# Kernel tuning notes

Measured on AMD Instinct MI355X. Metric: run time of the kernel, lower is better.

Reference implementation:

```python
import jax, jax.numpy as jnp
import numpy as np

ALPHA = 0.2  # LeakyReLU slope
EPS = 1e-16


def _spgat_layer(x, W, a, row, col, N, concat):
    # h: [N, d]
    h = x @ W
    d = h.shape[1]
    # edge attention: a^T [h_row || h_col]  (pyGAT SpGAT: exp(-leakyrelu(.)))
    f_src = h @ a[:d]   # [N]
    f_dst = h @ a[d:]   # [N]
    e = jnp.exp(-jax.nn.leaky_relu(f_src[row] + f_dst[col], ALPHA))  # [E]
    denom = jax.ops.segment_sum(e, row, num_segments=N) + EPS        # [N]
    num = jax.ops.segment_sum(e[:, None] * h[col], row, num_segments=N)  # [N, d]
    out = num / denom[:, None]
    return jax.nn.elu(out) if concat else out


def _spgat(x, W1, a1, W2, a2, edges):
    row, col = edges[0], edges[1]
    N = x.shape[0]
    h = _spgat_layer(x, W1, a1, row, col, N, concat=True)
    h = _spgat_layer(h, W2, a2, row, col, N, concat=False)
    return jax.nn.elu(h)


def setup_inputs() -> dict:
    key = jax.random.key(0)
    ks = jax.random.split(key, 20)
    VOCAB, NFEAT = 50000, 300
    N_TW, L = 50000, 16
    UV = 50000
    E = 800000
    HID, JOINT, NCLASS = 64, 128, 2
    B = 4096

    inp = {}
    # integer structure (constants)
    inp['features_index'] = jax.random.randint(ks[0], (N_TW, L), 0, VOCAB, dtype=jnp.int32)
    inp['tw_edges'] = jax.random.randint(ks[1], (2, E), 0, N_TW, dtype=jnp.int32)
    inp['ut_edges'] = jax.random.randint(ks[2], (2, E), 0, UV, dtype=jnp.int32)
    inp['tw_graph_idx'] = jax.random.randint(ks[3], (B,), 0, N_TW, dtype=jnp.int32)
    inp['ut_graph_idx'] = jax.random.randint(ks[4], (B,), 0, UV, dtype=jnp.int32)
    # learned parameters
    inp['word_emb'] = jax.random.normal(ks[5], (VOCAB, NFEAT), jnp.float32) * 0.1
    inp['user_emb'] = jax.random.normal(ks[6], (UV, NFEAT), jnp.float32) * 0.1
    def gat_params(k, din, dh, dout):
        k1, k2, k3, k4 = jax.random.split(k, 4)
        return (jax.random.normal(k1, (din, dh), jnp.float32) * (1.0 / np.sqrt(din)),
                jax.random.normal(k2, (2 * dh,), jnp.float32) * 0.1,
                jax.random.normal(k3, (dh, dout), jnp.float32) * (1.0 / np.sqrt(dh)),
                jax.random.normal(k4, (2 * dout,), jnp.float32) * 0.1)
    inp['tw_W1'], inp['tw_a1'], inp['tw_W2'], inp['tw_a2'] = gat_params(ks[7], NFEAT, HID, JOINT)
    inp['tu_W1'], inp['tu_a1'], inp['tu_W2'], inp['tu_a2'] = gat_params(ks[8], NFEAT, HID, JOINT)
    inp['weight_W'] = jax.random.uniform(ks[9], (JOINT, JOINT), jnp.float32, -0.1, 0.1)
    inp['weight_proj'] = jax.random.uniform(ks[10], (JOINT, 1), jnp.float32, -0.1, 0.1)
    inp['out_W'] = jax.random.normal(ks[11], (NCLASS, JOINT), jnp.float32) * (1.0 / np.sqrt(JOINT))
    inp['out_b'] = jnp.zeros((NCLASS,), jnp.float32)
    return inp


def reference(word_emb, user_emb, tw_W1, tw_a1, tw_W2, tw_a2,
              tu_W1, tu_a1, tu_W2, tu_a2, weight_W, weight_proj,
              out_W, out_b, features_index, tw_edges, ut_edges,
              tw_graph_idx, ut_graph_idx):
    # tweet features: mean of word embeddings per tweet  [N_tw, nfeat]
    twt_X = word_emb[features_index].mean(axis=1)
    tw_X = _spgat(twt_X, tw_W1, tw_a1, tw_W2, tw_a2, tw_edges)   # [N_tw, joint]
    tu_X = _spgat(user_emb, tu_W1, tu_a1, tu_W2, tu_a2, ut_edges)  # [uV, joint]
    # attention-weighted fusion of the two views
    u_tw = jnp.tanh(tw_X @ weight_W)
    u_tu = jnp.tanh(tu_X @ weight_W)
    att_tw = jnp.mean(u_tw @ weight_proj, axis=0)  # [1]
    att_tu = jnp.mean(u_tu @ weight_proj, axis=0)  # [1]
    att = jax.nn.softmax(jnp.concatenate([att_tw, att_tu], axis=0))  # [2]
    feat = att[0] * tw_X[tw_graph_idx] + att[1] * tu_X[ut_graph_idx]  # [B, joint]
    logits = feat @ out_W.T + out_b
    return jax.nn.log_softmax(logits, axis=1)
```

## Files before the change

kernel.cpp:

```cpp
#include <hip/hip_runtime.h>
#include <hip/hip_bf16.h>

typedef __hip_bfloat16 bf16;
typedef unsigned int uint32;
typedef __attribute__((ext_vector_type(8))) short s8v;
typedef __attribute__((ext_vector_type(4))) short s4v;
typedef __attribute__((ext_vector_type(8))) short bf8v;
typedef __attribute__((ext_vector_type(4))) float f4v;

#define CAP 64
#define CAPSH 6

__device__ __forceinline__ float waveReduce(float v) {
#pragma unroll
    for (int o = 32; o > 0; o >>= 1) v += __shfl_xor(v, o, 64);
    return v;
}

__device__ __forceinline__ short f2bf(float x) {
    __hip_bfloat16 h = __float2bfloat16(x);
    return *reinterpret_cast<short*>(&h);
}
__device__ __forceinline__ float bf2f(short s) {
    return __uint_as_float(((uint32)(unsigned short)s) << 16);
}
__device__ __forceinline__ uint32 pack2(float x, float y) {
    return (uint32)(unsigned short)f2bf(x) | (((uint32)(unsigned short)f2bf(y)) << 16);
}
__device__ __forceinline__ float blo(uint32 d) { return __uint_as_float(d << 16); }
__device__ __forceinline__ float bhi(uint32 d) { return __uint_as_float(d & 0xffff0000u); }
__device__ __forceinline__ float felu(float x) { return x > 0.f ? x : __expf(x) - 1.f; }

struct WJobs {
    const float* src[5];
    short* dst[5];
    int K[5], N[5], KP[5], total[5];
    int* cursor;
    float* attsum;
    int N2;
};
__global__ void wtrans_all(WJobs jb) {
    int j = blockIdx.y;
    int i = blockIdx.x * blockDim.x + threadIdx.x;
    if (j == 5) {
        if (i < jb.N2) jb.cursor[i] = i << CAPSH;
        if (i < 2) jb.attsum[i] = 0.f;
        return;
    }
    if (i >= jb.total[j]) return;
    int KP = jb.KP[j];
    int n = i / KP, k = i - n * KP;
    jb.dst[j][i] = f2bf(k < jb.K[j] ? jb.src[j][(size_t)k * jb.N[j] + n] : 0.f);
}

struct GJob {
    const void* A;
    const short* Wt;
    const float* av;
    void* C;
    float* fs;
    float* fd;
    int M;
};
struct SJob {
    const int* rowA; const int* colA;
    const int* rowB; const int* colB;
    int* cursor; int* ecol;
    int E; int NTW; int nbg; int Wsize;
};

template <typename AT, int K, int KPAD, int N, int CSTORE, bool DO_F, bool DO_ATT, bool DO_SCAT>
__global__ __launch_bounds__(256) void mfma_gemm(GJob j0, GJob j1, int nb0,
                                                 float* __restrict__ attsum, int bnd, SJob sj) {
    constexpr int NT = N / 16;
    constexpr int NP = KPAD / 64;
    int t = threadIdx.x;

    if constexpr (DO_SCAT) {
        if ((int)blockIdx.x >= sj.nbg) {
            int bb = (int)blockIdx.x - sj.nbg;
            int w = (int)blockIdx.x & 7;
            int i = (bb >> 3) * 256 + t;
            int lo = w * sj.Wsize;
            int hi = lo + sj.Wsize;
            int r = -1, c = 0;
            if (i < sj.E) {
                r = sj.rowA[i]; c = sj.colA[i];
            } else if (i < 2 * sj.E) {
                r = sj.NTW + sj.rowB[i - sj.E]; c = sj.colB[i - sj.E];
            }
            if (r >= lo && r < hi) {
                int p0 = atomicAdd(&sj.cursor[r], 1);
                if (p0 < (r << CAPSH) + CAP) sj.ecol[p0] = c;
            }
            return;
        }
    }

    __shared__ short As[64 * 72];
    __shared__ short Ws[N * 72];
    __shared__ float red[8];
    int lane = t & 63;
    int wid = t >> 6;
    int col = lane & 15;
    int quad = lane >> 4;

    int bid = blockIdx.x;
    bool sec = bid >= nb0;
    GJob J = sec ? j1 : j0;
    const AT* A = (const AT*)J.A;
    const short* Wt = J.Wt;
    const float* av = J.av;
    int M = J.M;
    int row0 = (sec ? bid - nb0 : bid) * 64;

    f4v acc[NT];
#pragma unroll
    for (int i = 0; i < NT; ++i) { f4v z = {0.f, 0.f, 0.f, 0.f}; acc[i] = z; }

    float4 ra[4];
    s8v rsa[2];
    s8v rb[NT / 2];

    auto issue = [&](int p) {
        int k0 = p * 64;
        if constexpr (sizeof(AT) == 4) {
            const float4* A4 = (const float4*)A;
            int f = t & 15, r0 = t >> 4;
#pragma unroll
            for (int r = 0; r < 4; ++r) {
                int gr = row0 + r0 + 16 * r;
                int f4i = (k0 >> 2) + f;
                float4 v = {0.f, 0.f, 0.f, 0.f};
                if (gr < M && f4i < K / 4) v = A4[(size_t)gr * (K / 4) + f4i];
                ra[r] = v;
            }
        } else {
            int c8 = t & 7, r0 = t >> 3;
#pragma unroll
            for (int r = 0; r < 2; ++r) {
                int gr = row0 + r0 + 32 * r;
                s8v v = {0, 0, 0, 0, 0, 0, 0, 0};
                if (gr < M) v = *(const s8v*)&A[(size_t)gr * K + k0 + c8 * 8];
                rsa[r] = v;
            }
        }
        {
            int c8 = t & 7, r0 = t >> 3;
#pragma unroll
            for (int r = 0; r < NT / 2; ++r)
                rb[r] = *(const s8v*)&Wt[(size_t)(r0 + 32 * r) * KPAD + k0 + c8 * 8];
        }
    };
    auto commit = [&]() {
        if constexpr (sizeof(AT) == 4) {
            int f = t & 15, r0 = t >> 4;
#pragma unroll
            for (int r = 0; r < 4; ++r) {
                float4 v = ra[r];
                s4v sv = {f2bf(v.x), f2bf(v.y), f2bf(v.z), f2bf(v.w)};
                *(s4v*)&As[(r0 + 16 * r) * 72 + f * 4] = sv;
            }
        } else {
            int c8 = t & 7, r0 = t >> 3;
#pragma unroll
            for (int r = 0; r < 2; ++r) *(s8v*)&As[(r0 + 32 * r) * 72 + c8 * 8] = rsa[r];
        }
        int c8 = t & 7, r0 = t >> 3;
#pragma unroll
        for (int r = 0; r < NT / 2; ++r) *(s8v*)&Ws[(r0 + 32 * r) * 72 + c8 * 8] = rb[r];
    };

    issue(0);
    for (int p = 0; p < NP; ++p) {
        __syncthreads();
        commit();
        __syncthreads();
        if (p + 1 < NP) issue(p + 1);
#pragma unroll
        for (int c2 = 0; c2 < 2; ++c2) {
            int ko = c2 * 32 + quad * 8;
            bf8v af = *(const bf8v*)&As[(wid * 16 + col) * 72 + ko];
#pragma unroll
            for (int nt = 0; nt < NT; ++nt) {
                bf8v bf = *(const bf8v*)&Ws[(nt * 16 + col) * 72 + ko];
                acc[nt] = __builtin_amdgcn_mfma_f32_16x16x32_bf16(af, bf, acc[nt], 0, 0, 0);
            }
        }
    }

    int mbase = row0 + wid * 16;
    if constexpr (CSTORE == 1) {
        float* C = (float*)J.C;
#pragma unroll
        for (int nt = 0; nt < NT; ++nt)
#pragma unroll
            for (int r = 0; r < 4; ++r) {
                int gr = mbase + quad * 4 + r;
                if (gr < M) C[(size_t)gr * N + nt * 16 + col] = acc[nt][r];
            }
    } else if constexpr (CSTORE == 2) {
        short* C = (short*)J.C;
#pragma unroll
        for (int nt = 0; nt < NT; ++nt)
#pragma unroll
            for (int r = 0; r < 4; ++r) {
                int gr = mbase + quad * 4 + r;
                if (gr < M) C[(size_t)gr * N + nt * 16 + col] = f2bf(acc[nt][r]);
            }
    }
    if constexpr (DO_F) {
        if (av) {
            float* fs = J.fs;
            float* fd = J.fd;
            float a0[NT], a1[NT];
#pragma unroll
            for (int nt = 0; nt < NT; ++nt) {
                a0[nt] = av[nt * 16 + col];
                a1[nt] = av[N + nt * 16 + col];
            }
#pragma unroll
            for (int r = 0; r < 4; ++r) {
                float p0 = 0.f, p1 = 0.f;
#pragma unroll
                for (int nt = 0; nt < NT; ++nt) {
                    p0 += acc[nt][r] * a0[nt];
                    p1 += acc[nt][r] * a1[nt];
                }
#pragma unroll
                for (int o = 8; o > 0; o >>= 1) {
                    p0 += __shfl_xor(p0, o, 64);
                    p1 += __shfl_xor(p1, o, 64);
                }
                int gr = mbase + quad * 4 + r;
                if (col == 0 && gr < M) { fs[gr] = p0; fd[gr] = p1; }
            }
        }
    }
    if constexpr (DO_ATT) {
        float s0 = 0.f, s1 = 0.f;
#pragma unroll
        for (int nt = 0; nt < NT; ++nt) {
            float pj = av[nt * 16 + col];
#pragma unroll
            for (int r = 0; r < 4; ++r) {
                int gr = mbase + quad * 4 + r;
                float v = tanhf(acc[nt][r]) * pj;
                if (gr < bnd) s0 += v; else s1 += v;
            }
        }
        s0 = waveReduce(s0);
        s1 = waveReduce(s1);
        if (lane == 0) { red[wid] = s0; red[4 + wid] = s1; }
        __syncthreads();
        if (t == 0) {
            atomicAdd(attsum + 0, red[0] + red[1] + red[2] + red[3]);
            atomicAdd(attsum + 1, red[4] + red[5] + red[6] + red[7]);
        }
    }
}

__global__ void gather_h64(const int* __restrict__ idx, const uint32* __restrict__ P,
                           const float* __restrict__ a,
                           short* __restrict__ H, float* __restrict__ fsv, float* __restrict__ fdv,
                           int N) {
    int wv = (blockIdx.x * blockDim.x + threadIdx.x) >> 6;
    int lane = threadIdx.x & 63;
    if (wv >= N) return;
    int hf = lane >> 5, li = lane & 31;
    const int* ip = idx + wv * 16;
    float a0 = 0.f, a1 = 0.f;
#pragma unroll
    for (int u = 0; u < 8; ++u) {
        int ind = ip[2 * u + hf];
        uint32 d = P[(size_t)ind * 32 + li];
        a0 += blo(d);
        a1 += bhi(d);
    }
    a0 += __shfl_xor(a0, 32, 64);
    a1 += __shfl_xor(a1, 32, 64);
    a0 *= 0.0625f;
    a1 *= 0.0625f;
    if (hf == 0) ((uint32*)H)[(size_t)wv * 32 + li] = pack2(a0, a1);
    float cp = hf ? 0.f : (a0 * a[2 * li] + a1 * a[2 * li + 1]);
    float cq = hf ? 0.f : (a0 * a[64 + 2 * li] + a1 * a[64 + 2 * li + 1]);
    float p = waveReduce(cp);
    float q = waveReduce(cq);
    if (lane == 0) { fsv[wv] = p; fdv[wv] = q; }
}

__global__ void agg64f_kernel(const int* __restrict__ cursor, const int* __restrict__ ecol,
                              const float* __restrict__ fs, const float* __restrict__ fd,
                              const uint32* __restrict__ hb, uint32* __restrict__ out,
                              int N2, int NTW) {
    int wv = (blockIdx.x * blockDim.x + threadIdx.x) >> 6;
    int lane = threadIdx.x & 63;
    if (wv >= N2) return;
    int s = wv << CAPSH;
    int ne = min(cursor[wv] - s, CAP);
    int coff = wv < NTW ? 0 : NTW;
    float fsr = fs[wv];
    int cl = 0;
    float el = 0.f;
    if (lane < ne) {
        cl = ecol[s + lane];
        float f = fsr + fd[coff + cl];
        el = __expf(-(f >= 0.f ? f : 0.2f * f));
    }
    int qd = lane >> 4, li = lane & 15;
    const uint2* h2 = (const uint2*)hb;
    float a0 = 0.f, a1 = 0.f, a2 = 0.f, a3 = 0.f, den = 0.f;
    for (int kb = 0; kb < ne; kb += 16) {
        int k0 = kb + qd, k1 = kb + 4 + qd, k2 = kb + 8 + qd, k3 = kb + 12 + qd;
        int c0 = __shfl(cl, k0, 64); float e0 = __shfl(el, k0, 64);
        int c1 = __shfl(cl, k1, 64); float e1 = __shfl(el, k1, 64);
        int c2 = __shfl(cl, k2, 64); float e2 = __shfl(el, k2, 64);
        int c3 = __shfl(cl, k3, 64); float e3 = __shfl(el, k3, 64);
        uint2 d0 = h2[(size_t)(coff + c0) * 16 + li];
        uint2 d1 = h2[(size_t)(coff + c1) * 16 + li];
        uint2 d2 = h2[(size_t)(coff + c2) * 16 + li];
        uint2 d3 = h2[(size_t)(coff + c3) * 16 + li];
        a0 += e0 * blo(d0.x) + e1 * blo(d1.x) + e2 * blo(d2.x) + e3 * blo(d3.x);
        a1 += e0 * bhi(d0.x) + e1 * bhi(d1.x) + e2 * bhi(d2.x) + e3 * bhi(d3.x);
        a2 += e0 * blo(d0.y) + e1 * blo(d1.y) + e2 * blo(d2.y) + e3 * blo(d3.y);
        a3 += e0 * bhi(d0.y) + e1 * bhi(d1.y) + e2 * bhi(d2.y) + e3 * bhi(d3.y);
        den += e0 + e1 + e2 + e3;
    }
    a0 += __shfl_xor(a0, 16, 64); a0 += __shfl_xor(a0, 32, 64);
    a1 += __shfl_xor(a1, 16, 64); a1 += __shfl_xor(a1, 32, 64);
    a2 += __shfl_xor(a2, 16, 64); a2 += __shfl_xor(a2, 32, 64);
    a3 += __shfl_xor(a3, 16, 64); a3 += __shfl_xor(a3, 32, 64);
    den += __shfl_xor(den, 16, 64); den += __shfl_xor(den, 32, 64);
    if (lane < 16) {
        float inv = 1.f / (den + 1e-16f);
        float v0 = felu(a0 * inv);
        float v1 = felu(a1 * inv);
        float v2 = felu(a2 * inv);
        float v3 = felu(a3 * inv);
        uint2 o = {pack2(v0, v1), pack2(v2, v3)};
        ((uint2*)out)[(size_t)wv * 16 + li] = o;
    }
}

__global__ void agg128f_kernel(const int* __restrict__ cursor, const int* __restrict__ ecol,
                               const float* __restrict__ fs, const float* __restrict__ fd,
                               const uint32* __restrict__ hb, uint32* __restrict__ out,
                               int N2, int NTW) {
    int wv = (blockIdx.x * blockDim.x + threadIdx.x) >> 6;
    int lane = threadIdx.x & 63;
    if (wv >= N2) return;
    int s = wv << CAPSH;
    int ne = min(cursor[wv] - s, CAP);
    int coff = wv < NTW ? 0 : NTW;
    float fsr = fs[wv];
    int cl = 0;
    float el = 0.f;
    if (lane < ne) {
        cl = ecol[s + lane];
        float f = fsr + fd[coff + cl];
        el = __expf(-(f >= 0.f ? f : 0.2f * f));
    }
    int hf = lane >> 5, li = lane & 31;
    const uint2* h2 = (const uint2*)hb;
    float a0 = 0.f, a1 = 0.f, a2 = 0.f, a3 = 0.f, den = 0.f;
    for (int kb = 0; kb < ne; kb += 8) {
        int k0 = kb + hf, k1 = kb + 2 + hf, k2 = kb + 4 + hf, k3 = kb + 6 + hf;
        int c0 = __shfl(cl, k0, 64); float e0 = __shfl(el, k0, 64);
        int c1 = __shfl(cl, k1, 64); float e1 = __shfl(el, k1, 64);
        int c2 = __shfl(cl, k2, 64); float e2 = __shfl(el, k2, 64);
        int c3 = __shfl(cl, k3, 64); float e3 = __shfl(el, k3, 64);
        uint2 d0 = h2[(size_t)(coff + c0) * 32 + li];
        uint2 d1 = h2[(size_t)(coff + c1) * 32 + li];
        uint2 d2 = h2[(size_t)(coff + c2) * 32 + li];
        uint2 d3 = h2[(size_t)(coff + c3) * 32 + li];
        a0 += e0 * blo(d0.x) + e1 * blo(d1.x) + e2 * blo(d2.x) + e3 * blo(d3.x);
        a1 += e0 * bhi(d0.x) + e1 * bhi(d1.x) + e2 * bhi(d2.x) + e3 * bhi(d3.x);
        a2 += e0 * blo(d0.y) + e1 * blo(d1.y) + e2 * blo(d2.y) + e3 * blo(d3.y);
        a3 += e0 * bhi(d0.y) + e1 * bhi(d1.y) + e2 * bhi(d2.y) + e3 * bhi(d3.y);
        den += e0 + e1 + e2 + e3;
    }
    a0 += __shfl_xor(a0, 32, 64);
    a1 += __shfl_xor(a1, 32, 64);
    a2 += __shfl_xor(a2, 32, 64);
    a3 += __shfl_xor(a3, 32, 64);
    den += __shfl_xor(den, 32, 64);
    if (hf == 0) {
        float inv = 1.f / (den + 1e-16f);
        float v0 = felu(a0 * inv);
        float v1 = felu(a1 * inv);
        float v2 = felu(a2 * inv);
        float v3 = felu(a3 * inv);
        uint2 o = {pack2(v0, v1), pack2(v2, v3)};
        ((uint2*)out)[(size_t)wv * 32 + li] = o;
    }
}

__global__ void final_kernel(const short* __restrict__ twX, const short* __restrict__ tuX,
                             const int* __restrict__ twi, const int* __restrict__ tui,
                             const float* __restrict__ attsum,
                             const float* __restrict__ outW, const float* __restrict__ outb,
                             float* __restrict__ out, int B, float invNtw, float invNuv) {
    int wave = (blockIdx.x * blockDim.x + threadIdx.x) >> 6;
    int lane = threadIdx.x & 63;
    if (wave >= B) return;
    float z0 = attsum[0] * invNtw, z1 = attsum[1] * invNuv;
    float m = fmaxf(z0, z1);
    float e0 = expf(z0 - m), e1 = expf(z1 - m);
    float a0 = e0 / (e0 + e1), a1 = e1 / (e0 + e1);
    int ti = twi[wave], ui = tui[wave];
    float l0 = 0.f, l1 = 0.f;
#pragma unroll
    for (int p = 0; p < 2; ++p) {
        int j = lane + 64 * p;
        float feat = a0 * bf2f(twX[(size_t)ti * 128 + j]) + a1 * bf2f(tuX[(size_t)ui * 128 + j]);
        l0 += feat * outW[j];
        l1 += feat * outW[128 + j];
    }
    l0 = waveReduce(l0);
    l1 = waveReduce(l1);
    if (lane == 0) {
        l0 += outb[0];
        l1 += outb[1];
        float mm = fmaxf(l0, l1);
        float lse = mm + logf(expf(l0 - mm) + expf(l1 - mm));
        out[wave * 2 + 0] = l0 - lse;
        out[wave * 2 + 1] = l1 - lse;
    }
}

extern "C" void kernel_launch(void* const* d_in, const int* in_sizes, int n_in,
                              void* d_out, int out_size, void* d_ws, size_t ws_size,
                              hipStream_t stream) {
    const int* features_index = (const int*)d_in[0];
    const int* tw_edges = (const int*)d_in[1];
    const int* ut_edges = (const int*)d_in[2];
    const int* tw_gidx = (const int*)d_in[3];
    const int* ut_gidx = (const int*)d_in[4];
    const float* word_emb = (const float*)d_in[5];
    const float* user_emb = (const float*)d_in[6];
    const float* tw_W1 = (const float*)d_in[7];
    const float* tw_a1 = (const float*)d_in[8];
    const float* tw_W2 = (const float*)d_in[9];
    const float* tw_a2 = (const float*)d_in[10];
    const float* tu_W1 = (const float*)d_in[11];
    const float* tu_a1 = (const float*)d_in[12];
    const float* tu_W2 = (const float*)d_in[13];
    const float* tu_a2 = (const float*)d_in[14];
    const float* weight_W = (const float*)d_in[15];
    const float* weight_proj = (const float*)d_in[16];
    const float* out_W = (const float*)d_in[17];
    const float* out_b = (const float*)d_in[18];

    const int E = in_sizes[1] / 2;
    const int NTW = in_sizes[0] / 16;
    const int VOCAB = in_sizes[5] / 300;
    const int UV = in_sizes[6] / 300;
    const int B = in_sizes[3];
    const int N2 = NTW + UV;

    char* ws = (char*)d_ws;
    size_t off = 0;
    auto carve = [&](size_t bytes) -> void* {
        void* p = ws + off;
        off += (bytes + 255) & ~(size_t)255;
        return p;
    };
    float* Pbuf = (float*)carve((size_t)VOCAB * 64 * sizeof(float));
    short* Hb1 = (short*)carve((size_t)N2 * 64 * sizeof(short));
    short* H2 = (short*)carve((size_t)N2 * 128 * sizeof(short));
    short* X = (short*)carve((size_t)N2 * 128 * sizeof(short));
    float* f_s = (float*)carve((size_t)N2 * sizeof(float));
    float* f_d = (float*)carve((size_t)N2 * sizeof(float));
    float* attsum = (float*)carve(256);
    int* cursor = (int*)carve((size_t)N2 * sizeof(int));
    int* ecol = (int*)carve((size_t)N2 * CAP * sizeof(int));
    short* Wt1tw = (short*)carve((size_t)64 * 320 * sizeof(short));
    short* Wt1tu = (short*)carve((size_t)64 * 320 * sizeof(short));
    short* Wt2tw = (short*)carve((size_t)128 * 64 * sizeof(short));
    short* Wt2tu = (short*)carve((size_t)128 * 64 * sizeof(short));
    short* Wta   = (short*)carve((size_t)128 * 128 * sizeof(short));
    short* num1 = ((size_t)VOCAB * 64 * sizeof(float) >= (size_t)N2 * 64 * sizeof(short))
                      ? (short*)Pbuf
                      : (short*)carve((size_t)N2 * 64 * sizeof(short));
    (void)ws_size; (void)n_in; (void)out_size;

    WJobs jb;
    jb.src[0] = tw_W1;    jb.dst[0] = Wt1tw; jb.K[0] = 300; jb.N[0] = 64;  jb.KP[0] = 320; jb.total[0] = 64 * 320;
    jb.src[1] = tu_W1;    jb.dst[1] = Wt1tu; jb.K[1] = 300; jb.N[1] = 64;  jb.KP[1] = 320; jb.total[1] = 64 * 320;
    jb.src[2] = tw_W2;    jb.dst[2] = Wt2tw; jb.K[2] = 64;  jb.N[2] = 128; jb.KP[2] = 64;  jb.total[2] = 128 * 64;
    jb.src[3] = tu_W2;    jb.dst[3] = Wt2tu; jb.K[3] = 64;  jb.N[3] = 128; jb.KP[3] = 64;  jb.total[3] = 128 * 64;
    jb.src[4] = weight_W; jb.dst[4] = Wta;   jb.K[4] = 128; jb.N[4] = 128; jb.KP[4] = 128; jb.total[4] = 128 * 128;
    jb.cursor = cursor;
    jb.attsum = attsum;
    jb.N2 = N2;
    {
        int gx = (64 * 320 + 255) / 256;
        int gc = (N2 + 255) / 256;
        if (gc > gx) gx = gc;
        dim3 g(gx, 6);
        wtrans_all<<<g, 256, 0, stream>>>(jb);
    }

    SJob sempty{nullptr, nullptr, nullptr, nullptr, nullptr, nullptr, 0, 0, 0, 0};

    {
        GJob a{word_emb, Wt1tw, nullptr, Pbuf, nullptr, nullptr, VOCAB};
        GJob b{user_emb, Wt1tu, tu_a1, Hb1 + (size_t)NTW * 64, f_s + NTW, f_d + NTW, UV};
        int nbw = (VOCAB + 63) / 64, nbu = (UV + 63) / 64;
        int nbg = nbw + nbu;
        int nsc = 8 * ((2 * E + 255) / 256);
        int Wsize = (N2 + 7) / 8;
        SJob sj{tw_edges, tw_edges + E, ut_edges, ut_edges + E, cursor, ecol, E, NTW, nbg, Wsize};
        mfma_gemm<float, 300, 320, 64, 2, true, false, true><<<nbg + nsc, 256, 0, stream>>>(
            a, b, nbw, nullptr, 0, sj);
    }
    gather_h64<<<(NTW + 3) / 4, 256, 0, stream>>>(features_index, (const uint32*)Pbuf, tw_a1,
                                                  Hb1, f_s, f_d, NTW);

    agg64f_kernel<<<(N2 + 3) / 4, 256, 0, stream>>>(cursor, ecol, f_s, f_d,
                                                    (const uint32*)Hb1, (uint32*)num1, N2, NTW);

    {
        int nbtw = (NTW + 63) / 64, nbtu = (UV + 63) / 64;
        GJob a{num1, Wt2tw, tw_a2, H2, f_s, f_d, NTW};
        GJob b{num1 + (size_t)NTW * 64, Wt2tu, tu_a2, H2 + (size_t)NTW * 128,
               f_s + NTW, f_d + NTW, UV};
        mfma_gemm<short, 64, 64, 128, 2, true, false, false><<<nbtw + nbtu, 256, 0, stream>>>(
            a, b, nbtw, nullptr, 0, sempty);
    }

    agg128f_kernel<<<(N2 + 3) / 4, 256, 0, stream>>>(cursor, ecol, f_s, f_d,
                                                     (const uint32*)H2, (uint32*)X, N2, NTW);

    {
        GJob a{X, Wta, weight_proj, nullptr, nullptr, nullptr, N2};
        int nb = (N2 + 63) / 64;
        mfma_gemm<short, 128, 128, 128, 0, false, true, false><<<nb, 256, 0, stream>>>(
            a, a, nb, attsum, NTW, sempty);
    }

    final_kernel<<<(B + 3) / 4, 256, 0, stream>>>(X, X + (size_t)NTW * 128, tw_gidx, ut_gidx,
                                                  attsum, out_W, out_b, (float*)d_out, B,
                                                  1.0f / (float)NTW, 1.0f / (float)UV);
}
```

Baseline: 435.8 us.

## Aggregate before second-layer GEMM using W2·a2 projections; split scatter kernel

Layer 2 is reordered by linearity. The attention logits are computed from the layer-1 output via precomputed W2·a2 vectors, inside the first aggregation kernel. The 64-wide features are then aggregated before being multiplied by W2, and ELU is fused into the GEMM store. This replaces a 128-wide edge gather with a 64-wide one and drops the H2 buffer, at the cost of bf16 rounding the aggregated value before the GEMM. The edge scatter also moves out of the fused GEMM launch into its own kernel.

```diff
diff --git a/kernel.cpp b/kernel.cpp
--- a/kernel.cpp
+++ b/kernel.cpp
@@ -37,6 +37,9 @@
     int K[5], N[5], KP[5], total[5];
     int* cursor;
     float* attsum;
+    float* vab;
+    const float* W2tw; const float* a2tw;
+    const float* W2tu; const float* a2tu;
     int N2;
 };
 __global__ void wtrans_all(WJobs jb) {
@@ -45,12 +48,42 @@
     if (j == 5) {
         if (i < jb.N2) jb.cursor[i] = i << CAPSH;
         if (i < 2) jb.attsum[i] = 0.f;
+        if (i < 256) {
+            int br = i >> 7;
+            int half = (i >> 6) & 1;
+            int k = i & 63;
+            const float* W2 = br ? jb.W2tu : jb.W2tw;
+            const float* a2 = br ? jb.a2tu : jb.a2tw;
+            float s = 0.f;
+#pragma unroll 4
+            for (int q = 0; q < 128; ++q) s += W2[k * 128 + q] * a2[half * 128 + q];
+            jb.vab[i] = s;
+        }
         return;
     }
     if (i >= jb.total[j]) return;
     int KP = jb.KP[j];
     int n = i / KP, k = i - n * KP;
     jb.dst[j][i] = f2bf(k < jb.K[j] ? jb.src[j][(size_t)k * jb.N[j] + n] : 0.f);
+}
+
+__global__ void scatter8_kernel(const int* __restrict__ rowA, const int* __restrict__ colA,
+                                const int* __restrict__ rowB, const int* __restrict__ colB,
+                                int* __restrict__ cursor, int* __restrict__ ecol,
+                                int E, int NTW, int Wsize) {
+    int w = (int)blockIdx.x & 7;
+    int i = ((int)blockIdx.x >> 3) * 256 + (int)threadIdx.x;
+    int lo = w * Wsize, hi = lo + Wsize;
+    int r = -1, c = 0;
+    if (i < E) {
+        r = rowA[i]; c = colA[i];
+    } else if (i < 2 * E) {
+        r = NTW + rowB[i - E]; c = colB[i - E];
+    }
+    if (r >= lo && r < hi) {
+        int p0 = atomicAdd(&cursor[r], 1);
+        if (p0 < (r << CAPSH) + CAP) ecol[p0] = c;
+    }
 }
 
 struct GJob {
@@ -62,40 +95,13 @@
     float* fd;
     int M;
 };
-struct SJob {
-    const int* rowA; const int* colA;
-    const int* rowB; const int* colB;
-    int* cursor; int* ecol;
-    int E; int NTW; int nbg; int Wsize;
-};
-
-template <typename AT, int K, int KPAD, int N, int CSTORE, bool DO_F, bool DO_ATT, bool DO_SCAT>
+
+template <typename AT, int K, int KPAD, int N, int CSTORE, bool DO_F, bool DO_ATT>
 __global__ __launch_bounds__(256) void mfma_gemm(GJob j0, GJob j1, int nb0,
-                                                 float* __restrict__ attsum, int bnd, SJob sj) {
+                                                 float* __restrict__ attsum, int bnd) {
     constexpr int NT = N / 16;
     constexpr int NP = KPAD / 64;
     int t = threadIdx.x;
-
-    if constexpr (DO_SCAT) {
-        if ((int)blockIdx.x >= sj.nbg) {
-            int bb = (int)blockIdx.x - sj.nbg;
-            int w = (int)blockIdx.x & 7;
-            int i = (bb >> 3) * 256 + t;
-            int lo = w * sj.Wsize;
-            int hi = lo + sj.Wsize;
-            int r = -1, c = 0;
-            if (i < sj.E) {
-                r = sj.rowA[i]; c = sj.colA[i];
-            } else if (i < 2 * sj.E) {
-                r = sj.NTW + sj.rowB[i - sj.E]; c = sj.colB[i - sj.E];
-            }
-            if (r >= lo && r < hi) {
-                int p0 = atomicAdd(&sj.cursor[r], 1);
-                if (p0 < (r << CAPSH) + CAP) sj.ecol[p0] = c;
-            }
-            return;
-        }
-    }
 
     __shared__ short As[64 * 72];
     __shared__ short Ws[N * 72];
@@ -199,14 +205,16 @@
                 int gr = mbase + quad * 4 + r;
                 if (gr < M) C[(size_t)gr * N + nt * 16 + col] = acc[nt][r];
             }
-    } else if constexpr (CSTORE == 2) {
+    } else if constexpr (CSTORE == 2 || CSTORE == 3) {
         short* C = (short*)J.C;
 #pragma unroll
         for (int nt = 0; nt < NT; ++nt)
 #pragma unroll
             for (int r = 0; r < 4; ++r) {
                 int gr = mbase + quad * 4 + r;
-                if (gr < M) C[(size_t)gr * N + nt * 16 + col] = f2bf(acc[nt][r]);
+                float v = acc[nt][r];
+                if constexpr (CSTORE == 3) v = felu(v);
+                if (gr < M) C[(size_t)gr * N + nt * 16 + col] = f2bf(v);
             }
     }
     if constexpr (DO_F) {
@@ -289,9 +297,12 @@
     if (lane == 0) { fsv[wv] = p; fdv[wv] = q; }
 }
 
-__global__ void agg64f_kernel(const int* __restrict__ cursor, const int* __restrict__ ecol,
+template <bool ELU, bool F2>
+__global__ void agg64t_kernel(const int* __restrict__ cursor, const int* __restrict__ ecol,
                               const float* __restrict__ fs, const float* __restrict__ fd,
                               const uint32* __restrict__ hb, uint32* __restrict__ out,
+                              const float* __restrict__ vab,
+                              float* __restrict__ fs2, float* __restrict__ fd2,
                               int N2, int NTW) {
     int wv = (blockIdx.x * blockDim.x + threadIdx.x) >> 6;
     int lane = threadIdx.x & 63;
@@ -331,67 +342,26 @@
     a2 += __shfl_xor(a2, 16, 64); a2 += __shfl_xor(a2, 32, 64);
     a3 += __shfl_xor(a3, 16, 64); a3 += __shfl_xor(a3, 32, 64);
     den += __shfl_xor(den, 16, 64); den += __shfl_xor(den, 32, 64);
+    float inv = 1.f / (den + 1e-16f);
+    float v0 = a0 * inv, v1 = a1 * inv, v2 = a2 * inv, v3 = a3 * inv;
+    if constexpr (ELU) {
+        v0 = felu(v0); v1 = felu(v1); v2 = felu(v2); v3 = felu(v3);
+    }
     if (lane < 16) {
-        float inv = 1.f / (den + 1e-16f);
-        float v0 = felu(a0 * inv);
-        float v1 = felu(a1 * inv);
-        float v2 = felu(a2 * inv);
-        float v3 = felu(a3 * inv);
         uint2 o = {pack2(v0, v1), pack2(v2, v3)};
         ((uint2*)out)[(size_t)wv * 16 + li] = o;
     }
-}
-
-__global__ void agg128f_kernel(const int* __restrict__ cursor, const int* __restrict__ ecol,
-                               const float* __restrict__ fs, const float* __restrict__ fd,
-                               const uint32* __restrict__ hb, uint32* __restrict__ out,
-                               int N2, int NTW) {
-    int wv = (blockIdx.x * blockDim.x + threadIdx.x) >> 6;
-    int lane = threadIdx.x & 63;
-    if (wv >= N2) return;
-    int s = wv << CAPSH;
-    int ne = min(cursor[wv] - s, CAP);
-    int coff = wv < NTW ? 0 : NTW;
-    float fsr = fs[wv];
-    int cl = 0;
-    float el = 0.f;
-    if (lane < ne) {
-        cl = ecol[s + lane];
-        float f = fsr + fd[coff + cl];
-        el = __expf(-(f >= 0.f ? f : 0.2f * f));
-    }
-    int hf = lane >> 5, li = lane & 31;
-    const uint2* h2 = (const uint2*)hb;
-    float a0 = 0.f, a1 = 0.f, a2 = 0.f, a3 = 0.f, den = 0.f;
-    for (int kb = 0; kb < ne; kb += 8) {
-        int k0 = kb + hf, k1 = kb + 2 + hf, k2 = kb + 4 + hf, k3 = kb + 6 + hf;
-        int c0 = __shfl(cl, k0, 64); float e0 = __shfl(el, k0, 64);
-        int c1 = __shfl(cl, k1, 64); float e1 = __shfl(el, k1, 64);
-        int c2 = __shfl(cl, k2, 64); float e2 = __shfl(el, k2, 64);
-        int c3 = __shfl(cl, k3, 64); float e3 = __shfl(el, k3, 64);
-        uint2 d0 = h2[(size_t)(coff + c0) * 32 + li];
-        uint2 d1 = h2[(size_t)(coff + c1) * 32 + li];
-        uint2 d2 = h2[(size_t)(coff + c2) * 32 + li];
-        uint2 d3 = h2[(size_t)(coff + c3) * 32 + li];
-        a0 += e0 * blo(d0.x) + e1 * blo(d1.x) + e2 * blo(d2.x) + e3 * blo(d3.x);
-        a1 += e0 * bhi(d0.x) + e1 * bhi(d1.x) + e2 * bhi(d2.x) + e3 * bhi(d3.x);
-        a2 += e0 * blo(d0.y) + e1 * blo(d1.y) + e2 * blo(d2.y) + e3 * blo(d3.y);
-        a3 += e0 * bhi(d0.y) + e1 * bhi(d1.y) + e2 * bhi(d2.y) + e3 * bhi(d3.y);
-        den += e0 + e1 + e2 + e3;
-    }
-    a0 += __shfl_xor(a0, 32, 64);
-    a1 += __shfl_xor(a1, 32, 64);
-    a2 += __shfl_xor(a2, 32, 64);
-    a3 += __shfl_xor(a3, 32, 64);
-    den += __shfl_xor(den, 32, 64);
-    if (hf == 0) {
-        float inv = 1.f / (den + 1e-16f);
-        float v0 = felu(a0 * inv);
-        float v1 = felu(a1 * inv);
-        float v2 = felu(a2 * inv);
-        float v3 = felu(a3 * inv);
-        uint2 o = {pack2(v0, v1), pack2(v2, v3)};
-        ((uint2*)out)[(size_t)wv * 32 + li] = o;
+    if constexpr (F2) {
+        const float* vv = vab + (wv < NTW ? 0 : 128);
+        float ps = 0.f, pd = 0.f;
+        if (lane < 16) {
+            ps = v0 * vv[4 * li] + v1 * vv[4 * li + 1] + v2 * vv[4 * li + 2] + v3 * vv[4 * li + 3];
+            pd = v0 * vv[64 + 4 * li] + v1 * vv[64 + 4 * li + 1] +
+                 v2 * vv[64 + 4 * li + 2] + v3 * vv[64 + 4 * li + 3];
+        }
+        ps = waveReduce(ps);
+        pd = waveReduce(pd);
+        if (lane == 0) { fs2[wv] = ps; fd2[wv] = pd; }
     }
 }
 
@@ -467,11 +437,14 @@
     };
     float* Pbuf = (float*)carve((size_t)VOCAB * 64 * sizeof(float));
     short* Hb1 = (short*)carve((size_t)N2 * 64 * sizeof(short));
-    short* H2 = (short*)carve((size_t)N2 * 128 * sizeof(short));
+    short* Y = (short*)carve((size_t)N2 * 64 * sizeof(short));
     short* X = (short*)carve((size_t)N2 * 128 * sizeof(short));
     float* f_s = (float*)carve((size_t)N2 * sizeof(float));
     float* f_d = (float*)carve((size_t)N2 * sizeof(float));
+    float* f_s2 = (float*)carve((size_t)N2 * sizeof(float));
+    float* f_d2 = (float*)carve((size_t)N2 * sizeof(float));
     float* attsum = (float*)carve(256);
+    float* vab = (float*)carve(256 * sizeof(float));
     int* cursor = (int*)carve((size_t)N2 * sizeof(int));
     int* ecol = (int*)carve((size_t)N2 * CAP * sizeof(int));
     short* Wt1tw = (short*)carve((size_t)64 * 320 * sizeof(short));
@@ -492,6 +465,9 @@
     jb.src[4] = weight_W; jb.dst[4] = Wta;   jb.K[4] = 128; jb.N[4] = 128; jb.KP[4] = 128; jb.total[4] = 128 * 128;
     jb.cursor = cursor;
     jb.attsum = attsum;
+    jb.vab = vab;
+    jb.W2tw = tw_W2; jb.a2tw = tw_a2;
+    jb.W2tu = tu_W2; jb.a2tu = tu_a2;
     jb.N2 = N2;
     {
         int gx = (64 * 320 + 255) / 256;
@@ -501,42 +477,44 @@
         wtrans_all<<<g, 256, 0, stream>>>(jb);
     }
 
-    SJob sempty{nullptr, nullptr, nullptr, nullptr, nullptr, nullptr, 0, 0, 0, 0};
+    {
+        int nchunk = (2 * E + 255) / 256;
+        int Wsize = (N2 + 7) / 8;
+        scatter8_kernel<<<8 * nchunk, 256, 0, stream>>>(tw_edges, tw_edges + E,
+                                                        ut_edges, ut_edges + E,
+                                                        cursor, ecol, E, NTW, Wsize);
+    }
 
     {
         GJob a{word_emb, Wt1tw, nullptr, Pbuf, nullptr, nullptr, VOCAB};
         GJob b{user_emb, Wt1tu, tu_a1, Hb1 + (size_t)NTW * 64, f_s + NTW, f_d + NTW, UV};
         int nbw = (VOCAB + 63) / 64, nbu = (UV + 63) / 64;
-        int nbg = nbw + nbu;
-        int nsc = 8 * ((2 * E + 255) / 256);
-        int Wsize = (N2 + 7) / 8;
-        SJob sj{tw_edges, tw_edges + E, ut_edges, ut_edges + E, cursor, ecol, E, NTW, nbg, Wsize};
-        mfma_gemm<float, 300, 320, 64, 2, true, false, true><<<nbg + nsc, 256, 0, stream>>>(
-            a, b, nbw, nullptr, 0, sj);
+        mfma_gemm<float, 300, 320, 64, 2, true, false><<<nbw + nbu, 256, 0, stream>>>(
+            a, b, nbw, nullptr, 0);
     }
     gather_h64<<<(NTW + 3) / 4, 256, 0, stream>>>(features_index, (const uint32*)Pbuf, tw_a1,
                                                   Hb1, f_s, f_d, NTW);
 
-    agg64f_kernel<<<(N2 + 3) / 4, 256, 0, stream>>>(cursor, ecol, f_s, f_d,
-                                                    (const uint32*)Hb1, (uint32*)num1, N2, NTW);
+    agg64t_kernel<true, true><<<(N2 + 3) / 4, 256, 0, stream>>>(
+        cursor, ecol, f_s, f_d, (const uint32*)Hb1, (uint32*)num1, vab, f_s2, f_d2, N2, NTW);
+
+    agg64t_kernel<false, false><<<(N2 + 3) / 4, 256, 0, stream>>>(
+        cursor, ecol, f_s2, f_d2, (const uint32*)num1, (uint32*)Y, nullptr, nullptr, nullptr,
+        N2, NTW);
 
     {
         int nbtw = (NTW + 63) / 64, nbtu = (UV + 63) / 64;
-        GJob a{num1, Wt2tw, tw_a2, H2, f_s, f_d, NTW};
-        GJob b{num1 + (size_t)NTW * 64, Wt2tu, tu_a2, H2 + (size_t)NTW * 128,
-               f_s + NTW, f_d + NTW, UV};
-        mfma_gemm<short, 64, 64, 128, 2, true, false, false><<<nbtw + nbtu, 256, 0, stream>>>(
-            a, b, nbtw, nullptr, 0, sempty);
-    }
-
-    agg128f_kernel<<<(N2 + 3) / 4, 256, 0, stream>>>(cursor, ecol, f_s, f_d,
-                                                     (const uint32*)H2, (uint32*)X, N2, NTW);
+        GJob a{Y, Wt2tw, nullptr, X, nullptr, nullptr, NTW};
+        GJob b{Y + (size_t)NTW * 64, Wt2tu, nullptr, X + (size_t)NTW * 128, nullptr, nullptr, UV};
+        mfma_gemm<short, 64, 64, 128, 3, false, false><<<nbtw + nbtu, 256, 0, stream>>>(
+            a, b, nbtw, nullptr, 0);
+    }
 
     {
         GJob a{X, Wta, weight_proj, nullptr, nullptr, nullptr, N2};
         int nb = (N2 + 63) / 64;
-        mfma_gemm<short, 128, 128, 128, 0, false, true, false><<<nb, 256, 0, stream>>>(
-            a, a, nb, attsum, NTW, sempty);
+        mfma_gemm<short, 128, 128, 128, 0, false, true><<<nb, 256, 0, stream>>>(
+            a, a, nb, attsum, NTW);
     }
 
     final_kernel<<<(B + 3) / 4, 256, 0, stream>>>(X, X + (size_t)NTW * 128, tw_gidx, ut_gidx,
```

Result: no change. 434.3 us (-0.3%).
